# Optimization experiments

Hardware: AMD Instinct MI355X
Metric: run time of the kernel (lower is better)

Reference implementation:

```python
import jax, jax.numpy as jnp
import numpy as np


def setup_inputs() -> dict:
    key = jax.random.key(0)
    x = jax.random.normal(key, (16384, 4096), dtype=jnp.float32)
    return {"x": x, "k": 64}


def reference(x, k):
    # allow_negative_topk=False -> select and output based on ReLU(x)
    scores = jax.nn.relu(x)                      # [N, D]
    kk = min(k, scores.shape[-1])
    _, topk_idx = jax.lax.top_k(scores, kk)      # [N, kk]
    rows = jnp.arange(scores.shape[0])[:, None]  # [N, 1]
    mask = jnp.zeros_like(scores).at[rows, topk_idx].set(1.0)
    return scores * mask
```

## Files before the change

kernel.cpp:

```cpp
#include <hip/hip_runtime.h>


constexpr int ROW_LEN = 4096;
constexpr int TPB     = 256;
constexpr int CAP     = 512;
constexpr unsigned int KPRE_BITS = 0x3FC00000u;

typedef float f32x4 __attribute__((ext_vector_type(4)));

__global__ __launch_bounds__(TPB, 4)
void topk_relu_kernel(const float* __restrict__ x, const int* __restrict__ kptr,
                      float* __restrict__ out, int rows)
{
    __shared__ unsigned int cand[CAP];
    __shared__ alignas(16) int hist[256];
    __shared__ int ccount;
    __shared__ unsigned int selT;
    __shared__ int selNeed;
    __shared__ unsigned long long wtot64[4];
    __shared__ int wtot[4];
    __shared__ int sel_digit, sel_kk, sel_flag;

    const int row = blockIdx.x;
    if (row >= rows) return;
    const int tid  = threadIdx.x;
    const int lane = tid & 63;
    const int wid  = tid >> 6;

    int k = *kptr;
    if (k > ROW_LEN) k = ROW_LEN;

    const float* __restrict__ xrow = x + (size_t)row * ROW_LEN;
    unsigned int key[16];
#pragma unroll
    for (int j = 0; j < 4; ++j) {
        f32x4 v = *(const f32x4*)(xrow + j * 1024 + tid * 4);
#pragma unroll
        for (int c = 0; c < 4; ++c)
            key[4 * j + c] = __float_as_uint(fmaxf(v[c], 0.0f));
    }

    if (tid == 0) ccount = 0;
    __syncthreads();

    int m = 0;
#pragma unroll
    for (int j = 0; j < 16; ++j) m += (key[j] > KPRE_BITS) ? 1 : 0;
    int inc = m;
#pragma unroll
    for (int d = 1; d < 64; d <<= 1) {
        int v = __shfl_up(inc, d);
        if (lane >= d) inc += v;
    }
    const int excl = inc - m;
    const int wt   = __shfl(inc, 63);
    int wb = 0;
    if (lane == 0) wb = atomicAdd(&ccount, wt);
    wb = __shfl(wb, 0);
    int pos = wb + excl;
#pragma unroll
    for (int j = 0; j < 16; ++j) {
        if (key[j] > KPRE_BITS) {
            if (pos < CAP) cand[pos] = key[j];
            ++pos;
        }
    }
    __syncthreads();
    const int cnt = ccount;

    unsigned int T;
    int need;

    if (cnt >= k && cnt <= CAP) {
        if (wid == 0) {
            unsigned int c[CAP / 64];
#pragma unroll
            for (int i = 0; i < CAP / 64; ++i) {
                const int idx = lane + 64 * i;
                c[i] = (idx < cnt) ? cand[idx] : 0u;
            }
            int kk = k;
            unsigned int prefix = 0;
#pragma unroll
            for (int p = 0; p < 4; ++p) {
                const int shift = 24 - 8 * p;
                ((int4*)hist)[lane] = make_int4(0, 0, 0, 0);
#pragma unroll
                for (int i = 0; i < CAP / 64; ++i) {
                    const int idx = lane + 64 * i;
                    const unsigned int ci = c[i];
                    if (idx < cnt && (p == 0 || (ci >> (shift + 8)) == prefix))
                        atomicAdd(&hist[(ci >> shift) & 255u], 1);
                }
                const int4 h = ((const int4*)hist)[lane];
                const int h0 = h.x, h1 = h.y, h2 = h.z, h3 = h.w;
                const int lsum = h0 + h1 + h2 + h3;
                int suf = lsum;
#pragma unroll
                for (int d = 1; d < 64; d <<= 1) {
                    int v = __shfl_down(suf, d);
                    if (lane < 64 - d) suf += v;
                }
                const unsigned long long mm = __ballot(suf >= kk);
                const int L = 63 - __clzll(mm);
                int dig = 0, kkn = 0;
                if (lane == L) {
                    int cum = suf - lsum;
                    const int hh[4] = {h0, h1, h2, h3};
#pragma unroll
                    for (int b = 3; b >= 0; --b) {
                        if (cum + hh[b] >= kk) { dig = lane * 4 + b; kkn = kk - cum; break; }
                        cum += hh[b];
                    }
                }
                dig = __shfl(dig, L);
                kk  = __shfl(kkn, L);
                prefix = (prefix << 8) | (unsigned int)dig;
            }
            if (lane == 0) { selT = prefix; selNeed = kk; }
        }
        __syncthreads();
        T = selT;
        need = selNeed;
    } else {
        int kk = k;
        unsigned int prefix = 0;
        int t0 = 0;
        for (int p = 0; p < 4; ++p) {
            const int shift = 24 - 8 * p;
            hist[tid] = 0;
            if (tid == 0) sel_flag = 0;
            __syncthreads();
#pragma unroll
            for (int j = 0; j < 16; ++j) {
                const unsigned int kj = key[j];
                if (kj != 0u && (p == 0 || (kj >> (shift + 8)) == prefix))
                    atomicAdd(&hist[(kj >> shift) & 255u], 1);
            }
            __syncthreads();
            if (tid < 64) {
                const int b0 = tid * 4;
                const int h0 = hist[b0 + 0], h1 = hist[b0 + 1];
                const int h2 = hist[b0 + 2], h3 = hist[b0 + 3];
                const int lsum = h0 + h1 + h2 + h3;
                int suf = lsum;
#pragma unroll
                for (int d = 1; d < 64; d <<= 1) {
                    int v = __shfl_down(suf, d);
                    if (lane < 64 - d) suf += v;
                }
                const unsigned long long mm = __ballot(suf >= kk);
                if (mm == 0ull) {
                    if (lane == 0) sel_flag = 1;
                } else {
                    const int L = 63 - __clzll(mm);
                    if (lane == L) {
                        int cum = suf - lsum;
                        const int hh[4] = {h0, h1, h2, h3};
#pragma unroll
                        for (int b = 3; b >= 0; --b) {
                            if (cum + hh[b] >= kk) { sel_digit = b0 + b; sel_kk = kk - cum; break; }
                            cum += hh[b];
                        }
                    }
                }
            }
            __syncthreads();
            if (sel_flag) { t0 = 1; break; }
            prefix = (prefix << 8) | (unsigned int)sel_digit;
            kk = sel_kk;
            __syncthreads();
        }
        if (t0) { T = 0u; need = 0; }
        else    { T = prefix; need = kk; }
    }

    unsigned long long packed = 0ull;
#pragma unroll
    for (int j = 0; j < 4; ++j) {
        int e = 0;
#pragma unroll
        for (int c = 0; c < 4; ++c) e += (key[4 * j + c] == T) ? 1 : 0;
        packed |= (unsigned long long)e << (16 * j);
    }
    unsigned long long incp = packed;
#pragma unroll
    for (int d = 1; d < 64; d <<= 1) {
        unsigned long long v = __shfl_up(incp, d);
        if (lane >= d) incp += v;
    }
    if (lane == 63) wtot64[wid] = incp;
    __syncthreads();
    unsigned long long base = 0ull;
    for (int w = 0; w < wid; ++w) base += wtot64[w];
    const unsigned long long exclp = base + incp - packed;
    const unsigned long long tot = wtot64[0] + wtot64[1] + wtot64[2] + wtot64[3];
    int S[4];
    S[0] = 0;
    S[1] = (int)(tot & 0xFFFFull);
    S[2] = S[1] + (int)((tot >> 16) & 0xFFFFull);
    S[3] = S[2] + (int)((tot >> 32) & 0xFFFFull);

    float* __restrict__ orow = out + (size_t)row * ROW_LEN;
#pragma unroll
    for (int j = 0; j < 4; ++j) {
        int rr = S[j] + (int)((exclp >> (16 * j)) & 0xFFFFull);
        f32x4 v;
#pragma unroll
        for (int c2 = 0; c2 < 4; ++c2) {
            const unsigned int kj = key[4 * j + c2];
            const bool eq = (kj == T);
            const bool keep = (kj > T) || (eq && rr < need);
            v[c2] = keep ? __uint_as_float(kj) : 0.0f;
            rr += eq ? 1 : 0;
        }
        *(f32x4*)(orow + j * 1024 + tid * 4) = v;
    }
}

extern "C" void kernel_launch(void* const* d_in, const int* in_sizes, int n_in,
                              void* d_out, int out_size, void* d_ws, size_t ws_size,
                              hipStream_t stream)
{
    const float* x    = (const float*)d_in[0];
    const int*   kptr = (const int*)d_in[1];
    float*       out  = (float*)d_out;
    const int rows = in_sizes[0] / ROW_LEN;
    topk_relu_kernel<<<rows, TPB, 0, stream>>>(x, kptr, out, rows);
}
```

Before: 100.9 us.

## Compact candidates per wave with ballot and select threshold redundantly in every wave

Candidate compaction now uses a per-wave ballot/mbcnt into a fixed 128-entry segment per wave, replacing the shuffle scan plus shared atomic counter. Each of the four waves then runs the radix threshold selection redundantly on its own private histogram. This removes the selT/selNeed broadcast and one block barrier, and stops three waves idling while wave 0 works. In exchange it repeats the selection work four times and falls back to the slow full-row path whenever any single wave holds more than 128 candidates.

```diff
diff --git a/kernel.cpp b/kernel.cpp
--- a/kernel.cpp
+++ b/kernel.cpp
@@ -3,6 +3,7 @@
 
 constexpr int ROW_LEN = 4096;
 constexpr int TPB     = 256;
+constexpr int SEG     = 128;
 constexpr int CAP     = 512;
 constexpr unsigned int KPRE_BITS = 0x3FC00000u;
 
@@ -12,13 +13,10 @@
 void topk_relu_kernel(const float* __restrict__ x, const int* __restrict__ kptr,
                       float* __restrict__ out, int rows)
 {
+    __shared__ alignas(16) int hist4[4][256];
     __shared__ unsigned int cand[CAP];
-    __shared__ alignas(16) int hist[256];
-    __shared__ int ccount;
-    __shared__ unsigned int selT;
-    __shared__ int selNeed;
+    __shared__ int scnt[4];
     __shared__ unsigned long long wtot64[4];
-    __shared__ int wtot[4];
     __shared__ int sel_digit, sel_kk, sel_flag;
 
     const int row = blockIdx.x;
@@ -40,89 +38,79 @@
             key[4 * j + c] = __float_as_uint(fmaxf(v[c], 0.0f));
     }
 
-    if (tid == 0) ccount = 0;
+    int base = 0;
+#pragma unroll
+    for (int j = 0; j < 16; ++j) {
+        const bool p = key[j] > KPRE_BITS;
+        const unsigned long long mask = __ballot(p);
+        const int prior = __builtin_amdgcn_mbcnt_hi(
+            (unsigned int)(mask >> 32),
+            __builtin_amdgcn_mbcnt_lo((unsigned int)mask, 0));
+        const int idx = base + prior;
+        if (p && idx < SEG) cand[(wid << 7) + idx] = key[j];
+        base += (int)__popcll(mask);
+    }
+    if (lane == 0) scnt[wid] = base;
     __syncthreads();
 
-    int m = 0;
-#pragma unroll
-    for (int j = 0; j < 16; ++j) m += (key[j] > KPRE_BITS) ? 1 : 0;
-    int inc = m;
-#pragma unroll
-    for (int d = 1; d < 64; d <<= 1) {
-        int v = __shfl_up(inc, d);
-        if (lane >= d) inc += v;
-    }
-    const int excl = inc - m;
-    const int wt   = __shfl(inc, 63);
-    int wb = 0;
-    if (lane == 0) wb = atomicAdd(&ccount, wt);
-    wb = __shfl(wb, 0);
-    int pos = wb + excl;
-#pragma unroll
-    for (int j = 0; j < 16; ++j) {
-        if (key[j] > KPRE_BITS) {
-            if (pos < CAP) cand[pos] = key[j];
-            ++pos;
-        }
-    }
-    __syncthreads();
-    const int cnt = ccount;
+    const int c0 = scnt[0], c1 = scnt[1], c2 = scnt[2], c3 = scnt[3];
+    const int cnt = c0 + c1 + c2 + c3;
+    const bool segok = (c0 <= SEG) & (c1 <= SEG) & (c2 <= SEG) & (c3 <= SEG);
 
     unsigned int T;
     int need;
 
-    if (cnt >= k && cnt <= CAP) {
-        if (wid == 0) {
-            unsigned int c[CAP / 64];
-#pragma unroll
-            for (int i = 0; i < CAP / 64; ++i) {
-                const int idx = lane + 64 * i;
-                c[i] = (idx < cnt) ? cand[idx] : 0u;
-            }
-            int kk = k;
-            unsigned int prefix = 0;
-#pragma unroll
-            for (int p = 0; p < 4; ++p) {
-                const int shift = 24 - 8 * p;
-                ((int4*)hist)[lane] = make_int4(0, 0, 0, 0);
-#pragma unroll
-                for (int i = 0; i < CAP / 64; ++i) {
-                    const int idx = lane + 64 * i;
-                    const unsigned int ci = c[i];
-                    if (idx < cnt && (p == 0 || (ci >> (shift + 8)) == prefix))
-                        atomicAdd(&hist[(ci >> shift) & 255u], 1);
+    if (cnt >= k && segok) {
+        const int sc[4] = {c0, c1, c2, c3};
+        unsigned int c[8];
+#pragma unroll
+        for (int i = 0; i < 8; ++i) {
+            const int s   = i >> 1;
+            const int off = lane + 64 * (i & 1);
+            c[i] = (off < sc[s]) ? cand[(s << 7) + off] : 0u;
+        }
+        int* __restrict__ myhist = &hist4[wid][0];
+        int kk = k;
+        unsigned int prefix = 0;
+#pragma unroll
+        for (int p = 0; p < 4; ++p) {
+            const int shift = 24 - 8 * p;
+            ((int4*)myhist)[lane] = make_int4(0, 0, 0, 0);
+#pragma unroll
+            for (int i = 0; i < 8; ++i) {
+                const unsigned int ci = c[i];
+                if (ci != 0u && (p == 0 || (ci >> (shift + 8)) == prefix))
+                    atomicAdd(&myhist[(ci >> shift) & 255u], 1);
+            }
+            const int4 h = ((const int4*)myhist)[lane];
+            const int h0 = h.x, h1 = h.y, h2 = h.z, h3 = h.w;
+            const int lsum = h0 + h1 + h2 + h3;
+            int suf = lsum;
+#pragma unroll
+            for (int d = 1; d < 64; d <<= 1) {
+                int v = __shfl_down(suf, d);
+                if (lane < 64 - d) suf += v;
+            }
+            const unsigned long long mm = __ballot(suf >= kk);
+            const int L = 63 - __clzll(mm);
+            int dig = 0, kkn = 0;
+            if (lane == L) {
+                int cum = suf - lsum;
+                const int hh[4] = {h0, h1, h2, h3};
+#pragma unroll
+                for (int b = 3; b >= 0; --b) {
+                    if (cum + hh[b] >= kk) { dig = lane * 4 + b; kkn = kk - cum; break; }
+                    cum += hh[b];
                 }
-                const int4 h = ((const int4*)hist)[lane];
-                const int h0 = h.x, h1 = h.y, h2 = h.z, h3 = h.w;
-                const int lsum = h0 + h1 + h2 + h3;
-                int suf = lsum;
-#pragma unroll
-                for (int d = 1; d < 64; d <<= 1) {
-                    int v = __shfl_down(suf, d);
-                    if (lane < 64 - d) suf += v;
-                }
-                const unsigned long long mm = __ballot(suf >= kk);
-                const int L = 63 - __clzll(mm);
-                int dig = 0, kkn = 0;
-                if (lane == L) {
-                    int cum = suf - lsum;
-                    const int hh[4] = {h0, h1, h2, h3};
-#pragma unroll
-                    for (int b = 3; b >= 0; --b) {
-                        if (cum + hh[b] >= kk) { dig = lane * 4 + b; kkn = kk - cum; break; }
-                        cum += hh[b];
-                    }
-                }
-                dig = __shfl(dig, L);
-                kk  = __shfl(kkn, L);
-                prefix = (prefix << 8) | (unsigned int)dig;
-            }
-            if (lane == 0) { selT = prefix; selNeed = kk; }
-        }
-        __syncthreads();
-        T = selT;
-        need = selNeed;
+            }
+            dig = __shfl(dig, L);
+            kk  = __shfl(kkn, L);
+            prefix = (prefix << 8) | (unsigned int)dig;
+        }
+        T = prefix;
+        need = kk;
     } else {
+        int* __restrict__ hist = &hist4[0][0];
         int kk = k;
         unsigned int prefix = 0;
         int t0 = 0;
@@ -191,9 +179,9 @@
     }
     if (lane == 63) wtot64[wid] = incp;
     __syncthreads();
-    unsigned long long base = 0ull;
-    for (int w = 0; w < wid; ++w) base += wtot64[w];
-    const unsigned long long exclp = base + incp - packed;
+    unsigned long long b64 = 0ull;
+    for (int w = 0; w < wid; ++w) b64 += wtot64[w];
+    const unsigned long long exclp = b64 + incp - packed;
     const unsigned long long tot = wtot64[0] + wtot64[1] + wtot64[2] + wtot64[3];
     int S[4];
     S[0] = 0;
```

Measured after the change: 112.5 us. 11.6% more time.
